# Performance work log

Measured on AMD Instinct MI355X. Metric: run time of the kernel, lower is better.

The kernel has to match this reference:

```python
import jax, jax.numpy as jnp
import numpy as np

BN_EPS = 1e-5
POOL_TARGETS = (1500, 750, 375)


def mesh_conv(x, nb, W, g, b):
    # x: (E, C), nb: (E, 4), W: (5*C, Cout)
    E, C = x.shape
    n = x[jnp.clip(nb, 0, E - 1)]              # (E, 4, C) gather
    p1 = jnp.sort(n[:, :2, :], axis=1)          # symmetrize face-pair 1
    p2 = jnp.sort(n[:, 2:, :], axis=1)          # symmetrize face-pair 2
    feat = jnp.concatenate([x, p1[:, 0], p1[:, 1], p2[:, 0], p2[:, 1]], axis=1)  # (E, 5C)
    h = feat @ W                                # (E, Cout)
    mu = h.mean(axis=0)
    var = h.var(axis=0)                         # biased var (BatchNorm training stats)
    h = (h - mu) * jax.lax.rsqrt(var + BN_EPS) * g + b
    return jax.nn.relu(h)


def mesh_pool(x, nb, target):
    E = x.shape[0]
    scores = jnp.linalg.norm(x, axis=1)
    keep = jnp.sort(jnp.argsort(-scores)[:target])          # (target,) sorted kept edges
    x_pool = x[keep]
    remap = jnp.full((E,), -1, dtype=jnp.int32).at[keep].set(jnp.arange(target, dtype=jnp.int32))
    nbr = remap[jnp.clip(nb[keep], 0, E - 1)]               # (target, 4)
    self_idx = jnp.broadcast_to(jnp.arange(target, dtype=jnp.int32)[:, None], nbr.shape)
    nb_pool = jnp.where(nbr < 0, self_idx, nbr)
    return x_pool, nb_pool, keep


def mesh_unpool(x_coarse, keep, E_fine):
    # keep is sorted ascending; nearest kept edge by integer index distance
    # (ties -> lower index, matching torch argmin-first semantics).
    idx = jnp.arange(E_fine)
    pos = jnp.searchsorted(keep, idx)
    K = keep.shape[0]
    left = jnp.clip(pos - 1, 0, K - 1)
    right = jnp.clip(pos, 0, K - 1)
    dl = jnp.abs(idx - keep[left])
    dr = jnp.abs(idx - keep[right])
    nn_idx = jnp.where(dl <= dr, left, right)
    return x_coarse[nn_idx]                                 # kept edges map to themselves (d=0)


def setup_inputs() -> dict:
    key = jax.random.key(0)
    ks = jax.random.split(key, 20)
    E = 200000
    x = jax.random.normal(ks[0], (E, 5), dtype=jnp.float32)
    nb = jax.random.randint(ks[1], (E, 4), 0, E, dtype=jnp.int64)

    def lin(k, cin, cout):
        return (jax.random.normal(k, (cin, cout), dtype=jnp.float32) * 0.05)

    dims = [(5, 64), (64, 128), (128, 256), (256, 512), (768, 256), (384, 128), (192, 64)]
    names = ['e1', 'e2', 'e3', 'e4', 'd3', 'd2', 'd1']
    inp = {'x': x, 'nb': nb}
    for i, ((cin, cout), nm) in enumerate(zip(dims, names)):
        inp['W_' + nm] = lin(ks[2 + i], cin * 5, cout)
        inp['g_' + nm] = jnp.ones((cout,), dtype=jnp.float32)
        inp['b_' + nm] = jnp.zeros((cout,), dtype=jnp.float32)
    inp['W_head'] = lin(ks[12], 64, 4)
    inp['bias_head'] = jnp.zeros((4,), dtype=jnp.float32)
    return inp


def _forward(x, nb,
             W_e1, g_e1, b_e1, W_e2, g_e2, b_e2, W_e3, g_e3, b_e3, W_e4, g_e4, b_e4,
             W_d3, g_d3, b_d3, W_d2, g_d2, b_d2, W_d1, g_d1, b_d1,
             W_head, bias_head):
    e1 = mesh_conv(x, nb, W_e1, g_e1, b_e1)
    e1p, nb1, keep1 = mesh_pool(e1, nb, POOL_TARGETS[0])
    e2 = mesh_conv(e1p, nb1, W_e2, g_e2, b_e2)
    e2p, nb2, keep2 = mesh_pool(e2, nb1, POOL_TARGETS[1])
    e3 = mesh_conv(e2p, nb2, W_e3, g_e3, b_e3)
    e3p, nb3, keep3 = mesh_pool(e3, nb2, POOL_TARGETS[2])
    e4 = mesh_conv(e3p, nb3, W_e4, g_e4, b_e4)
    d3 = mesh_unpool(e4, keep3, e3.shape[0])
    d3 = mesh_conv(jnp.concatenate([d3, e3], axis=1), nb2, W_d3, g_d3, b_d3)
    d2 = mesh_unpool(d3, keep2, e2.shape[0])
    d2 = mesh_conv(jnp.concatenate([d2, e2], axis=1), nb1, W_d2, g_d2, b_d2)
    d1 = mesh_unpool(d2, keep1, e1.shape[0])
    d1 = mesh_conv(jnp.concatenate([d1, e1], axis=1), nb, W_d1, g_d1, b_d1)
    return d1 @ W_head + bias_head


def reference(x, nb,
              W_e1, g_e1, b_e1, W_e2, g_e2, b_e2, W_e3, g_e3, b_e3, W_e4, g_e4, b_e4,
              W_d3, g_d3, b_d3, W_d2, g_d2, b_d2, W_d1, g_d1, b_d1,
              W_head, bias_head):
    return _forward(x, nb,
                    W_e1, g_e1, b_e1, W_e2, g_e2, b_e2, W_e3, g_e3, b_e3, W_e4, g_e4, b_e4,
                    W_d3, g_d3, b_d3, W_d2, g_d2, b_d2, W_d1, g_d1, b_d1,
                    W_head, bias_head)
```

## Files before the change

### kernel.cpp

```cpp
#include <hip/hip_runtime.h>
#include <stdint.h>

typedef unsigned long long u64;
typedef unsigned int u32;
typedef unsigned short ushort_t;

#define FI __device__ __forceinline__

static constexpr float BN_EPS_F = 1e-5f;
static constexpr int E0 = 200000;
static constexpr int T1 = 1500, T2 = 750, T3 = 375;
static constexpr int CAND_CAP = 4096;
static constexpr int NB_KEEP = (E0 + 1023) / 1024;

typedef __attribute__((ext_vector_type(8))) short short8;
typedef __attribute__((ext_vector_type(4))) float f32x4;

FI int iclampi(int v, int lo, int hi) { return v < lo ? lo : (v > hi ? hi : v); }

FI ushort_t f2b(float f) {
  u32 u = __float_as_uint(f);
  u32 r = (u + 0x7FFFu + ((u >> 16) & 1u)) >> 16;
  return (ushort_t)r;
}

FI int nearest_keep(const int* __restrict__ keep, int K, int idx) {
  int lo = 0, hi = K;
  while (lo < hi) { int mid = (lo + hi) >> 1; if (keep[mid] < idx) lo = mid + 1; else hi = mid; }
  int l = lo - 1; l = l < 0 ? 0 : (l > K - 1 ? K - 1 : l);
  int r = lo;     r = r < 0 ? 0 : (r > K - 1 ? K - 1 : r);
  int dl = idx - keep[l]; dl = dl < 0 ? -dl : dl;
  int dr = idx - keep[r]; dr = dr < 0 ? -dr : dr;
  return (dl <= dr) ? l : r;
}

FI int bsearch_eq(const int* __restrict__ keep, int K, int v) {
  int lo = 0, hi = K;
  while (lo < hi) { int mid = (lo + hi) >> 1; if (keep[mid] < v) lo = mid + 1; else hi = mid; }
  if (lo < K && keep[lo] == v) return lo;
  return -1;
}

template<int C, int Cout, int BR, int BC, int KT, int TR, int TC, int KSPLIT,
         bool FUSE_STATS>
__global__ __launch_bounds__((BR / TR) * (BC / TC))
void conv_kernel(const float* __restrict__ X,
                 const int* __restrict__ nb, int E,
                 const float* __restrict__ W,
                 float* __restrict__ H, float* __restrict__ stats)
{
  constexpr int NTH = (BR / TR) * (BC / TC);
  constexpr int VK = 5 * KT;
  constexpr int KC = C / KSPLIT;
  static_assert(KC % KT == 0, "KC % KT");

  const int row0 = blockIdx.x * BR;
  const int col0 = blockIdx.y * BC;
  const int c_begin = (KSPLIT > 1) ? (int)blockIdx.z * KC : 0;

  __shared__ float As[VK][BR];
  __shared__ float Bs[VK][BC];
  __shared__ int rowsS[5][BR];
  __shared__ float red[FUSE_STATS ? 2 * (BR / TR) * BC : 1];

  const int tid = threadIdx.x;

  for (int q = tid; q < BR; q += NTH) {
    int r = row0 + q;
    int rr[5];
    if (r < E) {
      rr[0] = r;
      #pragma unroll
      for (int j = 0; j < 4; j++) {
        int v = nb[(size_t)r * 4 + j];
        rr[1 + j] = iclampi(v, 0, E - 1);
      }
    } else {
      #pragma unroll
      for (int j = 0; j < 5; j++) rr[j] = -1;
    }
    #pragma unroll
    for (int j = 0; j < 5; j++) rowsS[j][q] = rr[j];
  }

  float acc[TR][TC];
  #pragma unroll
  for (int i = 0; i < TR; i++)
    #pragma unroll
    for (int j = 0; j < TC; j++) acc[i][j] = 0.f;

  const int tr = tid / (BC / TC);
  const int tc = tid % (BC / TC);
  const int rA = tr * TR;
  const int cB = tc * TC;

  for (int c0 = c_begin; c0 < c_begin + KC; c0 += KT) {
    __syncthreads();
    for (int q = tid; q < VK * (BC / 4); q += NTH) {
      int kk = q / (BC / 4);
      int c4 = q % (BC / 4);
      int p = kk / KT, t = kk % KT;
      float4 wv = *(const float4*)&W[(size_t)(p * C + c0 + t) * Cout + col0 + c4 * 4];
      *(float4*)&Bs[kk][c4 * 4] = wv;
    }
    for (int q = tid; q < BR * KT; q += NTH) {
      int t = q % KT, rq = q / KT;
      int c = c0 + t;
      float s0 = 0.f, a1 = 0.f, a2 = 0.f, a3 = 0.f, a4 = 0.f;
      if (rowsS[0][rq] >= 0) {
        float v0, v1, v2, v3;
        s0 = X[(size_t)rowsS[0][rq] * C + c];
        v0 = X[(size_t)rowsS[1][rq] * C + c];
        v1 = X[(size_t)rowsS[2][rq] * C + c];
        v2 = X[(size_t)rowsS[3][rq] * C + c];
        v3 = X[(size_t)rowsS[4][rq] * C + c];
        a1 = fminf(v0, v1); a2 = fmaxf(v0, v1);
        a3 = fminf(v2, v3); a4 = fmaxf(v2, v3);
      }
      As[0 * KT + t][rq] = s0;
      As[1 * KT + t][rq] = a1;
      As[2 * KT + t][rq] = a2;
      As[3 * KT + t][rq] = a3;
      As[4 * KT + t][rq] = a4;
    }
    __syncthreads();

    for (int kk = 0; kk < VK; kk++) {
      float a[TR], b[TC];
      #pragma unroll
      for (int i = 0; i < TR; i++) a[i] = As[kk][rA + i];
      #pragma unroll
      for (int j = 0; j < TC; j++) b[j] = Bs[kk][cB + j];
      #pragma unroll
      for (int i = 0; i < TR; i++)
        #pragma unroll
        for (int j = 0; j < TC; j++)
          acc[i][j] = fmaf(a[i], b[j], acc[i][j]);
    }
  }

  #pragma unroll
  for (int i = 0; i < TR; i++) {
    int r = row0 + rA + i;
    if (r < E) {
      if constexpr (KSPLIT > 1) {
        #pragma unroll
        for (int j = 0; j < TC; j++)
          atomicAdd(&H[(size_t)r * Cout + col0 + cB + j], acc[i][j]);
      } else {
        #pragma unroll
        for (int j = 0; j < TC; j += 4) {
          float4 v = make_float4(acc[i][j], acc[i][j + 1], acc[i][j + 2], acc[i][j + 3]);
          *(float4*)&H[(size_t)r * Cout + col0 + cB + j] = v;
        }
      }
    }
  }

  if constexpr (FUSE_STATS) {
    float s[TC], q2[TC];
    #pragma unroll
    for (int j = 0; j < TC; j++) { s[j] = 0.f; q2[j] = 0.f; }
    #pragma unroll
    for (int i = 0; i < TR; i++) {
      int r = row0 + rA + i;
      if (r < E) {
        #pragma unroll
        for (int j = 0; j < TC; j++) { float v = acc[i][j]; s[j] += v; q2[j] += v * v; }
      }
    }
    __syncthreads();
    float* redS = &red[0];
    float* redQ = &red[(BR / TR) * BC];
    #pragma unroll
    for (int j = 0; j < TC; j++) {
      redS[tr * BC + cB + j] = s[j];
      redQ[tr * BC + cB + j] = q2[j];
    }
    __syncthreads();
    for (int col = tid; col < BC; col += NTH) {
      float ts = 0.f, tq = 0.f;
      for (int g = 0; g < BR / TR; g++) { ts += redS[g * BC + col]; tq += redQ[g * BC + col]; }
      atomicAdd(&stats[col0 + col], ts);
      atomicAdd(&stats[Cout + col0 + col], tq);
    }
  }
}

__global__ __launch_bounds__(256)
void e1_conv_kernel(const float* __restrict__ X, const int* __restrict__ nb,
                    const float* __restrict__ W,
                    float* __restrict__ H, float* __restrict__ stats)
{
  __shared__ float As[25][128];
  __shared__ float Bs[25][64];
  __shared__ float red[2 * 32 * 64];

  const int tid = threadIdx.x;
  const int row0 = (int)blockIdx.x * 128;

  if (tid < 128) {
    int r = row0 + tid; if (r > E0 - 1) r = E0 - 1;
    int rs[5];
    rs[0] = r;
    #pragma unroll
    for (int j = 0; j < 4; j++) rs[1 + j] = iclampi((int)nb[(size_t)r * 4 + j], 0, E0 - 1);
    float v[5][5];
    #pragma unroll
    for (int j = 0; j < 5; j++) {
      const float* src = &X[(size_t)rs[j] * 5];
      float4 a = *(const float4*)src;
      v[j][0] = a.x; v[j][1] = a.y; v[j][2] = a.z; v[j][3] = a.w;
      v[j][4] = src[4];
    }
    #pragma unroll
    for (int c = 0; c < 5; c++) {
      As[0 * 5 + c][tid] = v[0][c];
      As[1 * 5 + c][tid] = fminf(v[1][c], v[2][c]);
      As[2 * 5 + c][tid] = fmaxf(v[1][c], v[2][c]);
      As[3 * 5 + c][tid] = fminf(v[3][c], v[4][c]);
      As[4 * 5 + c][tid] = fmaxf(v[3][c], v[4][c]);
    }
  } else {
    for (int q = tid - 128; q < 25 * 16; q += 128) {
      int k = q / 16, c4 = q % 16;
      float4 wv = *(const float4*)&W[(size_t)k * 64 + c4 * 4];
      *(float4*)&Bs[k][c4 * 4] = wv;
    }
  }
  __syncthreads();

  const int tr = tid >> 3;
  const int tc = tid & 7;
  const int rA = tr * 4;
  const int cB = tc * 8;

  float acc[4][8];
  #pragma unroll
  for (int i = 0; i < 4; i++)
    #pragma unroll
    for (int j = 0; j < 8; j++) acc[i][j] = 0.f;

  for (int k = 0; k < 25; k++) {
    float a[4], b[8];
    #pragma unroll
    for (int i = 0; i < 4; i++) a[i] = As[k][rA + i];
    #pragma unroll
    for (int j = 0; j < 8; j++) b[j] = Bs[k][cB + j];
    #pragma unroll
    for (int i = 0; i < 4; i++)
      #pragma unroll
      for (int j = 0; j < 8; j++)
        acc[i][j] = fmaf(a[i], b[j], acc[i][j]);
  }

  float s[8], q2[8];
  #pragma unroll
  for (int j = 0; j < 8; j++) { s[j] = 0.f; q2[j] = 0.f; }
  #pragma unroll
  for (int i = 0; i < 4; i++) {
    int r = row0 + rA + i;
    if (r < E0) {
      #pragma unroll
      for (int j = 0; j < 8; j += 4) {
        float4 v = make_float4(acc[i][j], acc[i][j + 1], acc[i][j + 2], acc[i][j + 3]);
        *(float4*)&H[(size_t)r * 64 + cB + j] = v;
      }
      #pragma unroll
      for (int j = 0; j < 8; j++) { float v = acc[i][j]; s[j] += v; q2[j] += v * v; }
    }
  }
  __syncthreads();
  float* redS = &red[0];
  float* redQ = &red[32 * 64];
  #pragma unroll
  for (int j = 0; j < 8; j++) {
    redS[tr * 64 + cB + j] = s[j];
    redQ[tr * 64 + cB + j] = q2[j];
  }
  __syncthreads();
  for (int col = tid; col < 64; col += 256) {
    float ts = 0.f, tq = 0.f;
    for (int g = 0; g < 32; g++) { ts += redS[g * 64 + col]; tq += redQ[g * 64 + col]; }
    atomicAdd(&stats[col], ts);
    atomicAdd(&stats[64 + col], tq);
  }
}

__global__ __launch_bounds__(256, 2)
void d1_mfma_kernel(const ushort_t* __restrict__ d2b, const ushort_t* __restrict__ e1b,
                    const int* __restrict__ nn1, const int* __restrict__ nb,
                    const ushort_t* __restrict__ Wt,
                    float* __restrict__ H, float* __restrict__ stats)
{
  __shared__ int rowsD[5][128];
  __shared__ int rowsS[5][128];

  const int tid = threadIdx.x;
  const int lane = tid & 63;
  const int wv = tid >> 6;
  const int l15 = lane & 15;
  const int quad = lane >> 4;
  const int row0 = (int)blockIdx.x * 128;

  if (tid < 128) {
    int r = row0 + tid; if (r > E0 - 1) r = E0 - 1;
    int rs[5];
    rs[0] = r;
    #pragma unroll
    for (int j = 0; j < 4; j++) rs[1 + j] = iclampi((int)nb[(size_t)r * 4 + j], 0, E0 - 1);
    #pragma unroll
    for (int j = 0; j < 5; j++) { rowsS[j][tid] = rs[j]; rowsD[j][tid] = nn1[rs[j]]; }
  }
  __syncthreads();

  f32x4 acc[2][4];
  #pragma unroll
  for (int mi = 0; mi < 2; mi++)
    #pragma unroll
    for (int ni = 0; ni < 4; ni++) acc[mi][ni] = (f32x4){0.f, 0.f, 0.f, 0.f};

  for (int cc = 0; cc < 6; cc++) {
    const bool fromD = cc < 4;
    const ushort_t* __restrict__ src = fromD ? d2b : e1b;
    const int stride = fromD ? 128 : 64;
    const int cbase = (fromD ? cc * 32 : (cc - 4) * 32) + quad * 8;

    short8 a[2][5];
    #pragma unroll
    for (int mi = 0; mi < 2; mi++) {
      int rr = wv * 32 + mi * 16 + l15;
      int r0, r1, r2, r3, r4;
      if (fromD) {
        r0 = rowsD[0][rr]; r1 = rowsD[1][rr]; r2 = rowsD[2][rr];
        r3 = rowsD[3][rr]; r4 = rowsD[4][rr];
      } else {
        r0 = rowsS[0][rr]; r1 = rowsS[1][rr]; r2 = rowsS[2][rr];
        r3 = rowsS[3][rr]; r4 = rowsS[4][rr];
      }
      uint4 v0 = *(const uint4*)&src[(size_t)r0 * stride + cbase];
      uint4 v1 = *(const uint4*)&src[(size_t)r1 * stride + cbase];
      uint4 v2 = *(const uint4*)&src[(size_t)r2 * stride + cbase];
      uint4 v3 = *(const uint4*)&src[(size_t)r3 * stride + cbase];
      uint4 v4 = *(const uint4*)&src[(size_t)r4 * stride + cbase];

      uint4 lo12, hi12, lo34, hi34;
      {
        const ushort_t* pa = (const ushort_t*)&v1;
        const ushort_t* pb = (const ushort_t*)&v2;
        ushort_t* lo = (ushort_t*)&lo12;
        ushort_t* hi = (ushort_t*)&hi12;
        #pragma unroll
        for (int i = 0; i < 8; i++) {
          ushort_t xx = pa[i], yy = pb[i];
          lo[i] = xx < yy ? xx : yy;
          hi[i] = xx < yy ? yy : xx;
        }
      }
      {
        const ushort_t* pa = (const ushort_t*)&v3;
        const ushort_t* pb = (const ushort_t*)&v4;
        ushort_t* lo = (ushort_t*)&lo34;
        ushort_t* hi = (ushort_t*)&hi34;
        #pragma unroll
        for (int i = 0; i < 8; i++) {
          ushort_t xx = pa[i], yy = pb[i];
          lo[i] = xx < yy ? xx : yy;
          hi[i] = xx < yy ? yy : xx;
        }
      }
      a[mi][0] = *(short8*)&v0;
      a[mi][1] = *(short8*)&lo12;
      a[mi][2] = *(short8*)&hi12;
      a[mi][3] = *(short8*)&lo34;
      a[mi][4] = *(short8*)&hi34;
    }

    #pragma unroll
    for (int p = 0; p < 5; p++) {
      short8 bf[4];
      #pragma unroll
      for (int ni = 0; ni < 4; ni++)
        bf[ni] = *(const short8*)&Wt[((size_t)(p * 64 + ni * 16 + l15)) * 192 + cc * 32 + quad * 8];
      #pragma unroll
      for (int mi = 0; mi < 2; mi++)
        #pragma unroll
        for (int ni = 0; ni < 4; ni++)
          acc[mi][ni] = __builtin_amdgcn_mfma_f32_16x16x32_bf16(a[mi][p], bf[ni], acc[mi][ni], 0, 0, 0);
    }
  }

  float s[4] = {0.f, 0.f, 0.f, 0.f}, q[4] = {0.f, 0.f, 0.f, 0.f};
  #pragma unroll
  for (int mi = 0; mi < 2; mi++) {
    #pragma unroll
    for (int reg = 0; reg < 4; reg++) {
      int r = row0 + wv * 32 + mi * 16 + quad * 4 + reg;
      if (r < E0) {
        #pragma unroll
        for (int ni = 0; ni < 4; ni++) {
          float v = acc[mi][ni][reg];
          H[(size_t)r * 64 + ni * 16 + l15] = v;
          s[ni] += v; q[ni] += v * v;
        }
      }
    }
  }
  #pragma unroll
  for (int ni = 0; ni < 4; ni++) {
    float ts = s[ni], tq = q[ni];
    ts += __shfl_xor(ts, 16); tq += __shfl_xor(tq, 16);
    ts += __shfl_xor(ts, 32); tq += __shfl_xor(tq, 32);
    if (quad == 0) {
      int col = ni * 16 + l15;
      atomicAdd(&stats[col], ts);
      atomicAdd(&stats[64 + col], tq);
    }
  }
}

__global__ void prep_wd1_kernel(const float* __restrict__ W, ushort_t* __restrict__ Wt)
{
  int idx = (int)blockIdx.x * 256 + threadIdx.x;
  if (idx < 5 * 64 * 192) {
    int n = idx & 63;
    int k = idx >> 6;
    int p = k / 192, c = k % 192;
    Wt[((size_t)(p * 64 + n)) * 192 + c] = f2b(W[(size_t)k * 64 + n]);
  }
}

__global__ void stats_kernel(const float* __restrict__ H, int E, int Cout,
                             float* __restrict__ stats)
{
  const int RB = 64;
  int r0 = (int)blockIdx.x * RB;
  int rend = r0 + RB; if (rend > E) rend = E;
  for (int col = threadIdx.x; col < Cout; col += blockDim.x) {
    float s = 0.f, q = 0.f;
    for (int r = r0; r < rend; r++) { float v = H[(size_t)r * Cout + col]; s += v; q += v * v; }
    atomicAdd(&stats[col], s);
    atomicAdd(&stats[Cout + col], q);
  }
}

template<int Cout, bool KEYS, bool B16>
__global__ void bn_kernel(const float* __restrict__ H, const float* __restrict__ stats,
                          const float* __restrict__ g, const float* __restrict__ b,
                          int E, float* __restrict__ Out, ushort_t* __restrict__ Outb,
                          u64* __restrict__ keys)
{
  constexpr int CPL = Cout / 64;
  const int lane = threadIdx.x & 63;
  const int wid = threadIdx.x >> 6;
  const int wpb = blockDim.x >> 6;
  const float invE = 1.0f / (float)E;
  float mu[CPL], inv[CPL], gg[CPL], bb[CPL];
  #pragma unroll
  for (int u = 0; u < CPL; u++) {
    int c = lane + u * 64;
    float m = stats[c] * invE;
    float var = stats[Cout + c] * invE - m * m;
    mu[u] = m;
    inv[u] = rsqrtf(var + BN_EPS_F);
    gg[u] = g[c]; bb[u] = b[c];
  }
  for (int r = (int)blockIdx.x * wpb + wid; r < E; r += (int)gridDim.x * wpb) {
    float ss = 0.f;
    #pragma unroll
    for (int u = 0; u < CPL; u++) {
      int c = lane + u * 64;
      float v = H[(size_t)r * Cout + c];
      float o = (v - mu[u]) * inv[u] * gg[u] + bb[u];
      o = fmaxf(o, 0.f);
      Out[(size_t)r * Cout + c] = o;
      if constexpr (B16) Outb[(size_t)r * Cout + c] = f2b(o);
      ss += o * o;
    }
    if constexpr (KEYS) {
      #pragma unroll
      for (int s = 32; s > 0; s >>= 1) ss += __shfl_xor(ss, s, 64);
      if (lane == 0) {
        float sc = sqrtf(ss);
        u32 sb = __float_as_uint(sc);
        keys[r] = ((u64)sb << 32) | (u64)(0xFFFFFFFFu - (u32)r);
      }
    }
  }
}

__global__ void head_kernel(const float* __restrict__ H, const float* __restrict__ stats,
                            const float* __restrict__ g, const float* __restrict__ b,
                            const float* __restrict__ Wh, const float* __restrict__ bh,
                            int E, float* __restrict__ out)
{
  const int lane = threadIdx.x & 63;
  const int wid = threadIdx.x >> 6;
  const int wpb = blockDim.x >> 6;
  const float invE = 1.0f / (float)E;
  float m = stats[lane] * invE;
  float var = stats[64 + lane] * invE - m * m;
  float inv = rsqrtf(var + BN_EPS_F);
  float gg = g[lane], bb = b[lane];
  float4 w = *(const float4*)&Wh[lane * 4];
  float b0 = bh[0], b1 = bh[1], b2 = bh[2], b3 = bh[3];
  for (int r = (int)blockIdx.x * wpb + wid; r < E; r += (int)gridDim.x * wpb) {
    float v = H[(size_t)r * 64 + lane];
    float o = fmaxf((v - m) * inv * gg + bb, 0.f);
    float a0 = o * w.x, a1 = o * w.y, a2 = o * w.z, a3 = o * w.w;
    #pragma unroll
    for (int s = 32; s > 0; s >>= 1) {
      a0 += __shfl_xor(a0, s, 64);
      a1 += __shfl_xor(a1, s, 64);
      a2 += __shfl_xor(a2, s, 64);
      a3 += __shfl_xor(a3, s, 64);
    }
    if (lane == 0) {
      float4 ov = make_float4(a0 + b0, a1 + b1, a2 + b2, a3 + b3);
      *(float4*)&out[(size_t)r * 4] = ov;
    }
  }
}

__global__ void hist_kernel(const u64* __restrict__ keys, int E, u32* __restrict__ hist)
{
  for (int i = (int)blockIdx.x * blockDim.x + threadIdx.x; i < E;
       i += (int)gridDim.x * blockDim.x) {
    u32 bin = (u32)(keys[i] >> 44);
    atomicAdd(&hist[bin], 1u);
  }
}

__global__ void scan_kernel(const u32* __restrict__ hist, int K, u32* __restrict__ sel)
{
  __shared__ u32 csum[1024];
  __shared__ u32 sb2[1024];
  __shared__ int selChunk;
  __shared__ u32 aboveChunk;
  const int tid = threadIdx.x;
  {
    const uint4* hp = (const uint4*)(hist + (size_t)tid * 1024);
    u32 s = 0;
    for (int i = 0; i < 256; i++) {
      uint4 v = hp[i];
      s += v.x + v.y + v.z + v.w;
    }
    csum[tid] = s;
  }
  __syncthreads();
  if (tid == 0) {
    u32 above = 0; int sc = 0; u32 ab = 0;
    for (int t = 1023; t >= 0; t--) {
      if (above + csum[t] >= (u32)K) { sc = t; ab = above; break; }
      above += csum[t];
    }
    selChunk = sc; aboveChunk = ab;
  }
  __syncthreads();
  sb2[tid] = hist[(size_t)selChunk * 1024 + tid];
  __syncthreads();
  if (tid == 0) {
    u32 above = aboveChunk; int sb = 0;
    for (int t = 1023; t >= 0; t--) {
      u32 c = sb2[t];
      if (above + c >= (u32)K) { sb = t; break; }
      above += c;
    }
    sel[0] = (u32)(selChunk * 1024 + sb);
    sel[1] = above;
    sel[2] = (u32)K - above;
  }
}

__global__ void collect_kernel(const u64* __restrict__ keys, int E, const u32* __restrict__ sel,
                               u64* __restrict__ cand, u32* __restrict__ count)
{
  u32 bin = sel[0];
  for (int i = (int)blockIdx.x * blockDim.x + threadIdx.x; i < E;
       i += (int)gridDim.x * blockDim.x) {
    if ((u32)(keys[i] >> 44) == bin) {
      u32 p = atomicAdd(count, 1u);
      if (p < (u32)CAND_CAP) cand[p] = keys[i];
    }
  }
}

__global__ void thresh_kernel(const u64* __restrict__ cand, const u32* __restrict__ count,
                              const u32* __restrict__ sel, u64* __restrict__ thr)
{
  __shared__ u64 sk[CAND_CAP];
  const int tid = threadIdx.x;
  const int nth = blockDim.x;
  int n = (int)(*count > (u32)CAND_CAP ? (u32)CAND_CAP : *count);
  int n2 = 2; while (n2 < n) n2 <<= 1;
  for (int i = tid; i < n2; i += nth) sk[i] = (i < n) ? cand[i] : 0ull;
  __syncthreads();
  for (int k = 2; k <= n2; k <<= 1)
    for (int j = k >> 1; j > 0; j >>= 1) {
      for (int i = tid; i < n2; i += nth) {
        int p = i ^ j;
        if (p > i) {
          u64 a = sk[i], bb = sk[p];
          bool up = ((i & k) == 0);
          bool sw = up ? (a < bb) : (a > bb);
          if (sw) { sk[i] = bb; sk[p] = a; }
        }
      }
      __syncthreads();
    }
  if (tid == 0) {
    int kr = (int)sel[2];
    thr[0] = sk[kr - 1];
  }
}

__global__ void keep_count_kernel(const u64* __restrict__ keys, int E,
                                  const u64* __restrict__ thrp, u32* __restrict__ bcnt)
{
  const u64 thr = thrp[0];
  const int tid = threadIdx.x;
  int base = (int)blockIdx.x * 1024 + tid * 4;
  u32 c = 0;
  #pragma unroll
  for (int u = 0; u < 4; u++) {
    int i = base + u;
    if (i < E && keys[i] >= thr) c++;
  }
  __shared__ u32 sm[256];
  sm[tid] = c;
  __syncthreads();
  for (int s = 128; s > 0; s >>= 1) {
    if (tid < s) sm[tid] += sm[tid + s];
    __syncthreads();
  }
  if (tid == 0) bcnt[blockIdx.x] = sm[0];
}

__global__ void keep_scan_kernel(const u32* __restrict__ bcnt, int NB, u32* __restrict__ boffs)
{
  __shared__ u32 sm[256];
  const int tid = threadIdx.x;
  u32 v = (tid < NB) ? bcnt[tid] : 0;
  sm[tid] = v;
  __syncthreads();
  for (int off = 1; off < 256; off <<= 1) {
    u32 t = 0;
    if (tid >= off) t = sm[tid - off];
    __syncthreads();
    sm[tid] += t;
    __syncthreads();
  }
  if (tid < NB) boffs[tid] = sm[tid] - v;
}

__global__ void keep_scatter_kernel(const u64* __restrict__ keys, int E,
                                    const u64* __restrict__ thrp, const u32* __restrict__ boffs,
                                    int* __restrict__ keep, int K)
{
  const u64 thr = thrp[0];
  const int tid = threadIdx.x;
  int base = (int)blockIdx.x * 1024 + tid * 4;
  u32 f[4]; u32 c = 0;
  #pragma unroll
  for (int u = 0; u < 4; u++) {
    int i = base + u;
    f[u] = (i < E && keys[i] >= thr) ? 1u : 0u;
    c += f[u];
  }
  __shared__ u32 sm[256];
  sm[tid] = c;
  __syncthreads();
  for (int off = 1; off < 256; off <<= 1) {
    u32 t = 0;
    if (tid >= off) t = sm[tid - off];
    __syncthreads();
    sm[tid] += t;
    __syncthreads();
  }
  u32 pos = boffs[blockIdx.x] + sm[tid] - c;
  #pragma unroll
  for (int u = 0; u < 4; u++) {
    if (f[u]) {
      if (pos < (u32)K) keep[pos] = base + u;
      pos++;
    }
  }
}

template<int NPOW>
__global__ void pool_select_kernel(const u64* __restrict__ keys, int E, int K,
                                   int* __restrict__ keep)
{
  __shared__ u64 sk[NPOW];
  __shared__ int si[NPOW];
  const int tid = threadIdx.x, nth = blockDim.x;
  for (int i = tid; i < NPOW; i += nth) sk[i] = (i < E) ? keys[i] : 0ull;
  __syncthreads();
  for (int k = 2; k <= NPOW; k <<= 1)
    for (int j = k >> 1; j > 0; j >>= 1) {
      for (int i = tid; i < NPOW; i += nth) {
        int p = i ^ j;
        if (p > i) {
          u64 a = sk[i], bb = sk[p];
          bool up = ((i & k) == 0);
          bool sw = up ? (a < bb) : (a > bb);
          if (sw) { sk[i] = bb; sk[p] = a; }
        }
      }
      __syncthreads();
    }
  for (int i = tid; i < NPOW; i += nth)
    si[i] = (i < K) ? (int)(0xFFFFFFFFu - (u32)(sk[i] & 0xFFFFFFFFull)) : 0x7FFFFFFF;
  __syncthreads();
  for (int k = 2; k <= NPOW; k <<= 1)
    for (int j = k >> 1; j > 0; j >>= 1) {
      for (int i = tid; i < NPOW; i += nth) {
        int p = i ^ j;
        if (p > i) {
          int a = si[i], bb = si[p];
          bool up = ((i & k) == 0);
          bool sw = up ? (a > bb) : (a < bb);
          if (sw) { si[i] = bb; si[p] = a; }
        }
      }
      __syncthreads();
    }
  for (int i = tid; i < K; i += nth) keep[i] = si[i];
}

template<int C>
__global__ void pool_finish_kernel(const float* __restrict__ Xsrc, const int* __restrict__ nb_src,
                                   const int* __restrict__ keep, int K, int Esrc,
                                   float* __restrict__ Xp, int* __restrict__ nbp)
{
  int total = K * C;
  for (int idx = (int)blockIdx.x * blockDim.x + threadIdx.x; idx < total;
       idx += (int)gridDim.x * blockDim.x) {
    int i = idx / C, c = idx % C;
    Xp[idx] = Xsrc[(size_t)keep[i] * C + c];
  }
  for (int idx = (int)blockIdx.x * blockDim.x + threadIdx.x; idx < K * 4;
       idx += (int)gridDim.x * blockDim.x) {
    int i = idx >> 2, j = idx & 3;
    int v = nb_src[(size_t)keep[i] * 4 + j];
    v = iclampi(v, 0, Esrc - 1);
    int p = bsearch_eq(keep, K, v);
    nbp[idx] = (p < 0) ? i : p;
  }
}

__global__ void unpool_cat_kernel(const float* __restrict__ Xc, const float* __restrict__ Xs,
                                  const int* __restrict__ keep, int K, int E,
                                  int Cc, int Cs, float* __restrict__ out)
{
  int Ct = Cc + Cs;
  int total = E * Ct;
  for (int idx = (int)blockIdx.x * blockDim.x + threadIdx.x; idx < total;
       idx += (int)gridDim.x * blockDim.x) {
    int r = idx / Ct, c = idx % Ct;
    float v;
    if (c < Cc) { int nn = nearest_keep(keep, K, r); v = Xc[(size_t)nn * Cc + c]; }
    else v = Xs[(size_t)r * Cs + (c - Cc)];
    out[idx] = v;
  }
}

__global__ void nn_map_kernel(const int* __restrict__ keep, int K, int E, int* __restrict__ nn)
{
  for (int i = (int)blockIdx.x * blockDim.x + threadIdx.x; i < E;
       i += (int)gridDim.x * blockDim.x)
    nn[i] = nearest_keep(keep, K, i);
}

extern "C" void kernel_launch(void* const* d_in, const int* in_sizes, int n_in,
                              void* d_out, int out_size, void* d_ws, size_t ws_size,
                              hipStream_t stream)
{
  (void)in_sizes; (void)n_in; (void)out_size; (void)ws_size;
  const float* x     = (const float*)d_in[0];
  const int*   nb    = (const int*)d_in[1];
  const float* W_e1  = (const float*)d_in[2];
  const float* g_e1  = (const float*)d_in[3];
  const float* b_e1  = (const float*)d_in[4];
  const float* W_e2  = (const float*)d_in[5];
  const float* g_e2  = (const float*)d_in[6];
  const float* b_e2  = (const float*)d_in[7];
  const float* W_e3  = (const float*)d_in[8];
  const float* g_e3  = (const float*)d_in[9];
  const float* b_e3  = (const float*)d_in[10];
  const float* W_e4  = (const float*)d_in[11];
  const float* g_e4  = (const float*)d_in[12];
  const float* b_e4  = (const float*)d_in[13];
  const float* W_d3  = (const float*)d_in[14];
  const float* g_d3  = (const float*)d_in[15];
  const float* b_d3  = (const float*)d_in[16];
  const float* W_d2  = (const float*)d_in[17];
  const float* g_d2  = (const float*)d_in[18];
  const float* b_d2  = (const float*)d_in[19];
  const float* W_d1  = (const float*)d_in[20];
  const float* g_d1  = (const float*)d_in[21];
  const float* b_d1  = (const float*)d_in[22];
  const float* W_head = (const float*)d_in[23];
  const float* bias_head = (const float*)d_in[24];
  float* out = (float*)d_out;

  char* p = (char*)d_ws;
  auto alloc = [&](size_t bytes) -> char* {
    char* q = p; p += (bytes + 255) & ~(size_t)255; return q;
  };

  char* zz = p;
  u32*   hist  = (u32*)alloc(sizeof(u32) * (1u << 20));
  float* stats = (float*)alloc(sizeof(float) * 2 * (64 + 128 + 256 + 512 + 256 + 128 + 64));
  u32*   ctrl  = (u32*)alloc(sizeof(u32) * 16);
  u64*   thr   = (u64*)alloc(sizeof(u64) * 2);
  u32*   sel   = (u32*)alloc(sizeof(u32) * 8);
  float* H2    = (float*)alloc(sizeof(float) * T1 * 128);
  float* H3    = (float*)alloc(sizeof(float) * T2 * 256);
  float* H4    = (float*)alloc(sizeof(float) * T3 * 512);
  float* Hd3   = (float*)alloc(sizeof(float) * T2 * 256);
  float* Hd2   = (float*)alloc(sizeof(float) * T1 * 128);
  size_t zz_bytes = (size_t)(p - zz);
  u32*   bcnt  = (u32*)alloc(sizeof(u32) * 256);
  u32*   boffs = (u32*)alloc(sizeof(u32) * 256);
  float* e1    = (float*)alloc(sizeof(float) * (size_t)E0 * 64);
  u64*   keys1 = (u64*)alloc(sizeof(u64) * E0);
  u64*   cand  = (u64*)alloc(sizeof(u64) * CAND_CAP);
  int*   keep1 = (int*)alloc(sizeof(int) * T1);
  float* e1p   = (float*)alloc(sizeof(float) * T1 * 64);
  int*   nb1   = (int*)alloc(sizeof(int) * T1 * 4);
  float* e2    = (float*)alloc(sizeof(float) * T1 * 128);
  u64*   keys2 = (u64*)alloc(sizeof(u64) * T1);
  int*   keep2 = (int*)alloc(sizeof(int) * T2);
  float* e2p   = (float*)alloc(sizeof(float) * T2 * 128);
  int*   nb2   = (int*)alloc(sizeof(int) * T2 * 4);
  float* e3    = (float*)alloc(sizeof(float) * T2 * 256);
  u64*   keys3 = (u64*)alloc(sizeof(u64) * T2);
  int*   keep3 = (int*)alloc(sizeof(int) * T3);
  float* e3p   = (float*)alloc(sizeof(float) * T3 * 256);
  int*   nb3   = (int*)alloc(sizeof(int) * T3 * 4);
  float* e4    = (float*)alloc(sizeof(float) * T3 * 512);
  float* d3cat = (float*)alloc(sizeof(float) * T2 * 768);
  float* d3    = (float*)alloc(sizeof(float) * T2 * 256);
  float* d2cat = (float*)alloc(sizeof(float) * T1 * 384);
  float* d2    = (float*)alloc(sizeof(float) * T1 * 128);
  int*   nn1   = (int*)alloc(sizeof(int) * E0);
  float* Hd1   = (float*)alloc(sizeof(float) * (size_t)E0 * 64);
  ushort_t* e1b = (ushort_t*)alloc(sizeof(ushort_t) * (size_t)E0 * 64);
  ushort_t* d2b = (ushort_t*)alloc(sizeof(ushort_t) * T1 * 128);
  ushort_t* Wt  = (ushort_t*)alloc(sizeof(ushort_t) * 5 * 64 * 192);

  float* s1  = stats;
  float* s2  = s1 + 2 * 64;
  float* s3  = s2 + 2 * 128;
  float* s4  = s3 + 2 * 256;
  float* sd3 = s4 + 2 * 512;
  float* sd2 = sd3 + 2 * 256;
  float* sd1 = sd2 + 2 * 128;

  hipMemsetAsync(zz, 0, zz_bytes, stream);
  prep_wd1_kernel<<<dim3(240), 256, 0, stream>>>(W_d1, Wt);

  e1_conv_kernel<<<dim3((E0 + 127) / 128), 256, 0, stream>>>(x, nb, W_e1, e1, s1);
  bn_kernel<64, true, true><<<dim3(8192), 256, 0, stream>>>(e1, s1, g_e1, b_e1, E0, e1, e1b, keys1);

  hist_kernel<<<dim3(782), 256, 0, stream>>>(keys1, E0, hist);
  scan_kernel<<<dim3(1), 1024, 0, stream>>>(hist, T1, sel);
  collect_kernel<<<dim3(782), 256, 0, stream>>>(keys1, E0, sel, cand, ctrl);
  thresh_kernel<<<dim3(1), 1024, 0, stream>>>(cand, ctrl, sel, thr);
  keep_count_kernel<<<dim3(NB_KEEP), 256, 0, stream>>>(keys1, E0, thr, bcnt);
  keep_scan_kernel<<<dim3(1), 256, 0, stream>>>(bcnt, NB_KEEP, boffs);
  keep_scatter_kernel<<<dim3(NB_KEEP), 256, 0, stream>>>(keys1, E0, thr, boffs, keep1, T1);
  pool_finish_kernel<64><<<dim3(380), 256, 0, stream>>>(e1, nb, keep1, T1, E0, e1p, nb1);

  conv_kernel<64, 128, 32, 64, 8, 2, 4, 2, false>
      <<<dim3((T1 + 31) / 32, 128 / 64, 2), 256, 0, stream>>>(e1p, nb1, T1, W_e2, H2, nullptr);
  stats_kernel<<<dim3((T1 + 63) / 64), 256, 0, stream>>>(H2, T1, 128, s2);
  bn_kernel<128, true, false><<<dim3(512), 256, 0, stream>>>(H2, s2, g_e2, b_e2, T1, e2, nullptr, keys2);
  pool_select_kernel<2048><<<dim3(1), 256, 0, stream>>>(keys2, T1, T2, keep2);
  pool_finish_kernel<128><<<dim3(380), 256, 0, stream>>>(e2, nb1, keep2, T2, T1, e2p, nb2);

  conv_kernel<128, 256, 32, 64, 8, 2, 4, 4, false>
      <<<dim3((T2 + 31) / 32, 256 / 64, 4), 256, 0, stream>>>(e2p, nb2, T2, W_e3, H3, nullptr);
  stats_kernel<<<dim3((T2 + 63) / 64), 256, 0, stream>>>(H3, T2, 256, s3);
  bn_kernel<256, true, false><<<dim3(256), 256, 0, stream>>>(H3, s3, g_e3, b_e3, T2, e3, nullptr, keys3);
  pool_select_kernel<1024><<<dim3(1), 256, 0, stream>>>(keys3, T2, T3, keep3);
  pool_finish_kernel<256><<<dim3(380), 256, 0, stream>>>(e3, nb2, keep3, T3, T2, e3p, nb3);

  conv_kernel<256, 512, 32, 64, 8, 2, 4, 4, false>
      <<<dim3((T3 + 31) / 32, 512 / 64, 4), 256, 0, stream>>>(e3p, nb3, T3, W_e4, H4, nullptr);
  stats_kernel<<<dim3((T3 + 63) / 64), 256, 0, stream>>>(H4, T3, 512, s4);
  bn_kernel<512, false, false><<<dim3(128), 256, 0, stream>>>(H4, s4, g_e4, b_e4, T3, e4, nullptr, nullptr);

  unpool_cat_kernel<<<dim3((T2 * 768 + 255) / 256), 256, 0, stream>>>(
      e4, e3, keep3, T3, T2, 512, 256, d3cat);
  conv_kernel<768, 256, 32, 64, 8, 2, 4, 8, false>
      <<<dim3((T2 + 31) / 32, 256 / 64, 8), 256, 0, stream>>>(d3cat, nb2, T2, W_d3, Hd3, nullptr);
  stats_kernel<<<dim3((T2 + 63) / 64), 256, 0, stream>>>(Hd3, T2, 256, sd3);
  bn_kernel<256, false, false><<<dim3(256), 256, 0, stream>>>(Hd3, sd3, g_d3, b_d3, T2, d3, nullptr, nullptr);

  unpool_cat_kernel<<<dim3((T1 * 384 + 255) / 256), 256, 0, stream>>>(
      d3, e2, keep2, T2, T1, 256, 128, d2cat);
  conv_kernel<384, 128, 32, 64, 8, 2, 4, 8, false>
      <<<dim3((T1 + 31) / 32, 128 / 64, 8), 256, 0, stream>>>(d2cat, nb1, T1, W_d2, Hd2, nullptr);
  stats_kernel<<<dim3((T1 + 63) / 64), 256, 0, stream>>>(Hd2, T1, 128, sd2);
  bn_kernel<128, false, true><<<dim3(512), 256, 0, stream>>>(Hd2, sd2, g_d2, b_d2, T1, d2, d2b, nullptr);

  nn_map_kernel<<<dim3(782), 256, 0, stream>>>(keep1, T1, E0, nn1);
  d1_mfma_kernel<<<dim3((E0 + 127) / 128), 256, 0, stream>>>(d2b, e1b, nn1, nb, Wt, Hd1, sd1);

  head_kernel<<<dim3(8192), 256, 0, stream>>>(Hd1, sd1, g_d1, b_d1, W_head, bias_head, E0, out);
}
```

Baseline: 1.194 ms.

## Move e4/d3/d2 convs to bf16 MFMA kernel with fused stats; prefetch d1 gathers

Adds a templated bf16 MFMA mesh-conv kernel that gathers bf16 rows, symmetrises neighbour pairs with u16 min/max and accumulates per-column BN statistics in the epilogue. It replaces the fp32 split-K conv plus separate stats kernels for e4, d3 and d2. Pool-finish and unpool-concat now write bf16 inputs, and new prep kernels transpose and convert those weights. The d1 kernel double-buffers its gathered rows so the next chunk loads while the current one computes. The cost is extra weight-conversion launches per call, bf16 rounding on these layers, and no split-K, so the small-E layers get fewer blocks.

```diff
diff --git a/kernel.cpp b/kernel.cpp
--- a/kernel.cpp
+++ b/kernel.cpp
@@ -22,6 +22,19 @@
   u32 u = __float_as_uint(f);
   u32 r = (u + 0x7FFFu + ((u >> 16) & 1u)) >> 16;
   return (ushort_t)r;
+}
+
+FI void u16minmax(const uint4& va, const uint4& vb, uint4& lo, uint4& hi) {
+  const ushort_t* a = (const ushort_t*)&va;
+  const ushort_t* b = (const ushort_t*)&vb;
+  ushort_t* l = (ushort_t*)&lo;
+  ushort_t* h = (ushort_t*)&hi;
+  #pragma unroll
+  for (int i = 0; i < 8; i++) {
+    ushort_t x = a[i], y = b[i];
+    l[i] = x < y ? x : y;
+    h[i] = x < y ? y : x;
+  }
 }
 
 FI int nearest_keep(const int* __restrict__ keep, int K, int idx) {
@@ -287,6 +300,102 @@
   }
 }
 
+template<int C, int Cout>
+__global__ __launch_bounds__(128)
+void mfma_conv_kernel(const ushort_t* __restrict__ src,
+                      const int* __restrict__ nb, int E,
+                      const ushort_t* __restrict__ Wt,
+                      float* __restrict__ H, float* __restrict__ stats)
+{
+  constexpr int NCC = C / 32;
+  __shared__ int rows[5][32];
+
+  const int tid = threadIdx.x;
+  const int lane = tid & 63;
+  const int wv = tid >> 6;
+  const int l15 = lane & 15;
+  const int quad = lane >> 4;
+  const int row0 = (int)blockIdx.x * 32;
+  const int col0 = (int)blockIdx.y * 64;
+
+  if (tid < 32) {
+    int r = row0 + tid; if (r > E - 1) r = E - 1;
+    rows[0][tid] = r;
+    #pragma unroll
+    for (int j = 0; j < 4; j++) rows[1 + j][tid] = iclampi(nb[(size_t)r * 4 + j], 0, E - 1);
+  }
+  __syncthreads();
+
+  const int rr = wv * 16 + l15;
+  int r5[5];
+  #pragma unroll
+  for (int j = 0; j < 5; j++) r5[j] = rows[j][rr];
+
+  f32x4 acc[4];
+  #pragma unroll
+  for (int ni = 0; ni < 4; ni++) acc[ni] = (f32x4){0.f, 0.f, 0.f, 0.f};
+
+  uint4 raw[2][5];
+  auto loadcc = [&](int par, int cc2) {
+    int cb = cc2 * 32 + quad * 8;
+    #pragma unroll
+    for (int j = 0; j < 5; j++)
+      raw[par][j] = *(const uint4*)&src[(size_t)r5[j] * C + cb];
+  };
+
+  loadcc(0, 0);
+  #pragma unroll
+  for (int cc = 0; cc < NCC; cc++) {
+    const int par = cc & 1;
+    if (cc + 1 < NCC) loadcc(par ^ 1, cc + 1);
+    short8 a[5];
+    a[0] = *(short8*)&raw[par][0];
+    {
+      uint4 lo, hi;
+      u16minmax(raw[par][1], raw[par][2], lo, hi);
+      a[1] = *(short8*)&lo; a[2] = *(short8*)&hi;
+    }
+    {
+      uint4 lo, hi;
+      u16minmax(raw[par][3], raw[par][4], lo, hi);
+      a[3] = *(short8*)&lo; a[4] = *(short8*)&hi;
+    }
+    #pragma unroll
+    for (int p = 0; p < 5; p++) {
+      #pragma unroll
+      for (int ni = 0; ni < 4; ni++) {
+        short8 bf = *(const short8*)&Wt[((size_t)(p * Cout + col0 + ni * 16 + l15)) * C + cc * 32 + quad * 8];
+        acc[ni] = __builtin_amdgcn_mfma_f32_16x16x32_bf16(a[p], bf, acc[ni], 0, 0, 0);
+      }
+    }
+  }
+
+  float s[4] = {0.f, 0.f, 0.f, 0.f}, q[4] = {0.f, 0.f, 0.f, 0.f};
+  #pragma unroll
+  for (int reg = 0; reg < 4; reg++) {
+    int r = row0 + wv * 16 + quad * 4 + reg;
+    if (r < E) {
+      #pragma unroll
+      for (int ni = 0; ni < 4; ni++) {
+        float v = acc[ni][reg];
+        H[(size_t)r * Cout + col0 + ni * 16 + l15] = v;
+        s[ni] += v; q[ni] += v * v;
+      }
+    }
+  }
+  #pragma unroll
+  for (int ni = 0; ni < 4; ni++) {
+    float ts = s[ni], tq = q[ni];
+    ts += __shfl_xor(ts, 16); tq += __shfl_xor(tq, 16);
+    ts += __shfl_xor(ts, 32); tq += __shfl_xor(tq, 32);
+    if (quad == 0) {
+      int col = col0 + ni * 16 + l15;
+      atomicAdd(&stats[col], ts);
+      atomicAdd(&stats[Cout + col], tq);
+    }
+  }
+}
+
 __global__ __launch_bounds__(256, 2)
 void d1_mfma_kernel(const ushort_t* __restrict__ d2b, const ushort_t* __restrict__ e1b,
                     const int* __restrict__ nn1, const int* __restrict__ nb,
@@ -314,68 +423,55 @@
   }
   __syncthreads();
 
+  int rD[2][5], rS[2][5];
+  #pragma unroll
+  for (int mi = 0; mi < 2; mi++) {
+    int rr = wv * 32 + mi * 16 + l15;
+    #pragma unroll
+    for (int j = 0; j < 5; j++) { rD[mi][j] = rowsD[j][rr]; rS[mi][j] = rowsS[j][rr]; }
+  }
+
   f32x4 acc[2][4];
   #pragma unroll
   for (int mi = 0; mi < 2; mi++)
     #pragma unroll
     for (int ni = 0; ni < 4; ni++) acc[mi][ni] = (f32x4){0.f, 0.f, 0.f, 0.f};
 
+  uint4 raw[2][2][5];
+  auto loadcc = [&](int par, int cc2) {
+    const bool fD = cc2 < 4;
+    const ushort_t* s2 = fD ? d2b : e1b;
+    const int st = fD ? 128 : 64;
+    const int cb = (fD ? cc2 * 32 : (cc2 - 4) * 32) + quad * 8;
+    #pragma unroll
+    for (int mi = 0; mi < 2; mi++)
+      #pragma unroll
+      for (int j = 0; j < 5; j++) {
+        int r = fD ? rD[mi][j] : rS[mi][j];
+        raw[par][mi][j] = *(const uint4*)&s2[(size_t)r * st + cb];
+      }
+  };
+
+  loadcc(0, 0);
+  #pragma unroll
   for (int cc = 0; cc < 6; cc++) {
-    const bool fromD = cc < 4;
-    const ushort_t* __restrict__ src = fromD ? d2b : e1b;
-    const int stride = fromD ? 128 : 64;
-    const int cbase = (fromD ? cc * 32 : (cc - 4) * 32) + quad * 8;
-
+    const int par = cc & 1;
+    if (cc + 1 < 6) loadcc(par ^ 1, cc + 1);
     short8 a[2][5];
     #pragma unroll
     for (int mi = 0; mi < 2; mi++) {
-      int rr = wv * 32 + mi * 16 + l15;
-      int r0, r1, r2, r3, r4;
-      if (fromD) {
-        r0 = rowsD[0][rr]; r1 = rowsD[1][rr]; r2 = rowsD[2][rr];
-        r3 = rowsD[3][rr]; r4 = rowsD[4][rr];
-      } else {
-        r0 = rowsS[0][rr]; r1 = rowsS[1][rr]; r2 = rowsS[2][rr];
-        r3 = rowsS[3][rr]; r4 = rowsS[4][rr];
-      }
-      uint4 v0 = *(const uint4*)&src[(size_t)r0 * stride + cbase];
-      uint4 v1 = *(const uint4*)&src[(size_t)r1 * stride + cbase];
-      uint4 v2 = *(const uint4*)&src[(size_t)r2 * stride + cbase];
-      uint4 v3 = *(const uint4*)&src[(size_t)r3 * stride + cbase];
-      uint4 v4 = *(const uint4*)&src[(size_t)r4 * stride + cbase];
-
-      uint4 lo12, hi12, lo34, hi34;
+      a[mi][0] = *(short8*)&raw[par][mi][0];
       {
-        const ushort_t* pa = (const ushort_t*)&v1;
-        const ushort_t* pb = (const ushort_t*)&v2;
-        ushort_t* lo = (ushort_t*)&lo12;
-        ushort_t* hi = (ushort_t*)&hi12;
-        #pragma unroll
-        for (int i = 0; i < 8; i++) {
-          ushort_t xx = pa[i], yy = pb[i];
-          lo[i] = xx < yy ? xx : yy;
-          hi[i] = xx < yy ? yy : xx;
-        }
+        uint4 lo, hi;
+        u16minmax(raw[par][mi][1], raw[par][mi][2], lo, hi);
+        a[mi][1] = *(short8*)&lo; a[mi][2] = *(short8*)&hi;
       }
       {
-        const ushort_t* pa = (const ushort_t*)&v3;
-        const ushort_t* pb = (const ushort_t*)&v4;
-        ushort_t* lo = (ushort_t*)&lo34;
-        ushort_t* hi = (ushort_t*)&hi34;
-        #pragma unroll
-        for (int i = 0; i < 8; i++) {
-          ushort_t xx = pa[i], yy = pb[i];
-          lo[i] = xx < yy ? xx : yy;
-          hi[i] = xx < yy ? yy : xx;
-        }
-      }
-      a[mi][0] = *(short8*)&v0;
-      a[mi][1] = *(short8*)&lo12;
-      a[mi][2] = *(short8*)&hi12;
-      a[mi][3] = *(short8*)&lo34;
-      a[mi][4] = *(short8*)&hi34;
-    }
-
+        uint4 lo, hi;
+        u16minmax(raw[par][mi][3], raw[par][mi][4], lo, hi);
+        a[mi][3] = *(short8*)&lo; a[mi][4] = *(short8*)&hi;
+      }
+    }
     #pragma unroll
     for (int p = 0; p < 5; p++) {
       short8 bf[4];
@@ -419,14 +515,15 @@
   }
 }
 
-__global__ void prep_wd1_kernel(const float* __restrict__ W, ushort_t* __restrict__ Wt)
+template<int C, int Cout>
+__global__ void prep_w_kernel(const float* __restrict__ W, ushort_t* __restrict__ Wt)
 {
   int idx = (int)blockIdx.x * 256 + threadIdx.x;
-  if (idx < 5 * 64 * 192) {
-    int n = idx & 63;
-    int k = idx >> 6;
-    int p = k / 192, c = k % 192;
-    Wt[((size_t)(p * 64 + n)) * 192 + c] = f2b(W[(size_t)k * 64 + n]);
+  if (idx < 5 * C * Cout) {
+    int n = idx % Cout;
+    int k = idx / Cout;
+    int p = k / C, c = k % C;
+    Wt[((size_t)(p * Cout + n)) * C + c] = f2b(W[(size_t)k * Cout + n]);
   }
 }
 
@@ -728,16 +825,19 @@
   for (int i = tid; i < K; i += nth) keep[i] = si[i];
 }
 
-template<int C>
+template<int C, bool B16>
 __global__ void pool_finish_kernel(const float* __restrict__ Xsrc, const int* __restrict__ nb_src,
                                    const int* __restrict__ keep, int K, int Esrc,
-                                   float* __restrict__ Xp, int* __restrict__ nbp)
+                                   float* __restrict__ Xp, ushort_t* __restrict__ Xpb,
+                                   int* __restrict__ nbp)
 {
   int total = K * C;
   for (int idx = (int)blockIdx.x * blockDim.x + threadIdx.x; idx < total;
        idx += (int)gridDim.x * blockDim.x) {
     int i = idx / C, c = idx % C;
-    Xp[idx] = Xsrc[(size_t)keep[i] * C + c];
+    float v = Xsrc[(size_t)keep[i] * C + c];
+    if constexpr (B16) Xpb[idx] = f2b(v);
+    else Xp[idx] = v;
   }
   for (int idx = (int)blockIdx.x * blockDim.x + threadIdx.x; idx < K * 4;
        idx += (int)gridDim.x * blockDim.x) {
@@ -749,9 +849,9 @@
   }
 }
 
-__global__ void unpool_cat_kernel(const float* __restrict__ Xc, const float* __restrict__ Xs,
-                                  const int* __restrict__ keep, int K, int E,
-                                  int Cc, int Cs, float* __restrict__ out)
+__global__ void unpool_cat_b16_kernel(const float* __restrict__ Xc, const float* __restrict__ Xs,
+                                      const int* __restrict__ keep, int K, int E,
+                                      int Cc, int Cs, ushort_t* __restrict__ out)
 {
   int Ct = Cc + Cs;
   int total = E * Ct;
@@ -761,7 +861,7 @@
     float v;
     if (c < Cc) { int nn = nearest_keep(keep, K, r); v = Xc[(size_t)nn * Cc + c]; }
     else v = Xs[(size_t)r * Cs + (c - Cc)];
-    out[idx] = v;
+    out[idx] = f2b(v);
   }
 }
 
@@ -817,10 +917,10 @@
   u32*   sel   = (u32*)alloc(sizeof(u32) * 8);
   float* H2    = (float*)alloc(sizeof(float) * T1 * 128);
   float* H3    = (float*)alloc(sizeof(float) * T2 * 256);
+  size_t zz_bytes = (size_t)(p - zz);
   float* H4    = (float*)alloc(sizeof(float) * T3 * 512);
   float* Hd3   = (float*)alloc(sizeof(float) * T2 * 256);
   float* Hd2   = (float*)alloc(sizeof(float) * T1 * 128);
-  size_t zz_bytes = (size_t)(p - zz);
   u32*   bcnt  = (u32*)alloc(sizeof(u32) * 256);
   u32*   boffs = (u32*)alloc(sizeof(u32) * 256);
   float* e1    = (float*)alloc(sizeof(float) * (size_t)E0 * 64);
@@ -837,18 +937,21 @@
   float* e3    = (float*)alloc(sizeof(float) * T2 * 256);
   u64*   keys3 = (u64*)alloc(sizeof(u64) * T2);
   int*   keep3 = (int*)alloc(sizeof(int) * T3);
-  float* e3p   = (float*)alloc(sizeof(float) * T3 * 256);
+  ushort_t* e3pb = (ushort_t*)alloc(sizeof(ushort_t) * T3 * 256);
   int*   nb3   = (int*)alloc(sizeof(int) * T3 * 4);
   float* e4    = (float*)alloc(sizeof(float) * T3 * 512);
-  float* d3cat = (float*)alloc(sizeof(float) * T2 * 768);
+  ushort_t* d3catb = (ushort_t*)alloc(sizeof(ushort_t) * T2 * 768);
   float* d3    = (float*)alloc(sizeof(float) * T2 * 256);
-  float* d2cat = (float*)alloc(sizeof(float) * T1 * 384);
+  ushort_t* d2catb = (ushort_t*)alloc(sizeof(ushort_t) * T1 * 384);
   float* d2    = (float*)alloc(sizeof(float) * T1 * 128);
   int*   nn1   = (int*)alloc(sizeof(int) * E0);
   float* Hd1   = (float*)alloc(sizeof(float) * (size_t)E0 * 64);
   ushort_t* e1b = (ushort_t*)alloc(sizeof(ushort_t) * (size_t)E0 * 64);
   ushort_t* d2b = (ushort_t*)alloc(sizeof(ushort_t) * T1 * 128);
-  ushort_t* Wt  = (ushort_t*)alloc(sizeof(ushort_t) * 5 * 64 * 192);
+  ushort_t* Wt1 = (ushort_t*)alloc(sizeof(ushort_t) * 5 * 64 * 192);
+  ushort_t* Wt4 = (ushort_t*)alloc(sizeof(ushort_t) * 5 * 512 * 256);
+  ushort_t* Wtd3 = (ushort_t*)alloc(sizeof(ushort_t) * 5 * 256 * 768);
+  ushort_t* Wtd2 = (ushort_t*)alloc(sizeof(ushort_t) * 5 * 128 * 384);
 
   float* s1  = stats;
   float* s2  = s1 + 2 * 64;
@@ -859,7 +962,10 @@
   float* sd1 = sd2 + 2 * 128;
 
   hipMemsetAsync(zz, 0, zz_bytes, stream);
-  prep_wd1_kernel<<<dim3(240), 256, 0, stream>>>(W_d1, Wt);
+  prep_w_kernel<192, 64><<<dim3((5 * 192 * 64 + 255) / 256), 256, 0, stream>>>(W_d1, Wt1);
+  prep_w_kernel<256, 512><<<dim3((5 * 256 * 512 + 255) / 256), 256, 0, stream>>>(W_e4, Wt4);
+  prep_w_kernel<768, 256><<<dim3((5 * 768 * 256 + 255) / 256), 256, 0, stream>>>(W_d3, Wtd3);
+  prep_w_kernel<384, 128><<<dim3((5 * 384 * 128 + 255) / 256), 256, 0, stream>>>(W_d2, Wtd2);
 
   e1_conv_kernel<<<dim3((E0 + 127) / 128), 256, 0, stream>>>(x, nb, W_e1, e1, s1);
   bn_kernel<64, true, true><<<dim3(8192), 256, 0, stream>>>(e1, s1, g_e1, b_e1, E0, e1, e1b, keys1);
@@ -871,43 +977,40 @@
   keep_count_kernel<<<dim3(NB_KEEP), 256, 0, stream>>>(keys1, E0, thr, bcnt);
   keep_scan_kernel<<<dim3(1), 256, 0, stream>>>(bcnt, NB_KEEP, boffs);
   keep_scatter_kernel<<<dim3(NB_KEEP), 256, 0, stream>>>(keys1, E0, thr, boffs, keep1, T1);
-  pool_finish_kernel<64><<<dim3(380), 256, 0, stream>>>(e1, nb, keep1, T1, E0, e1p, nb1);
+  pool_finish_kernel<64, false><<<dim3(380), 256, 0, stream>>>(e1, nb, keep1, T1, E0, e1p, nullptr, nb1);
 
   conv_kernel<64, 128, 32, 64, 8, 2, 4, 2, false>
       <<<dim3((T1 + 31) / 32, 128 / 64, 2), 256, 0, stream>>>(e1p, nb1, T1, W_e2, H2, nullptr);
   stats_kernel<<<dim3((T1 + 63) / 64), 256, 0, stream>>>(H2, T1, 128, s2);
   bn_kernel<128, true, false><<<dim3(512), 256, 0, stream>>>(H2, s2, g_e2, b_e2, T1, e2, nullptr, keys2);
   pool_select_kernel<2048><<<dim3(1), 256, 0, stream>>>(keys2, T1, T2, keep2);
-  pool_finish_kernel<128><<<dim3(380), 256, 0, stream>>>(e2, nb1, keep2, T2, T1, e2p, nb2);
+  pool_finish_kernel<128, false><<<dim3(380), 256, 0, stream>>>(e2, nb1, keep2, T2, T1, e2p, nullptr, nb2);
 
   conv_kernel<128, 256, 32, 64, 8, 2, 4, 4, false>
       <<<dim3((T2 + 31) / 32, 256 / 64, 4), 256, 0, stream>>>(e2p, nb2, T2, W_e3, H3, nullptr);
   stats_kernel<<<dim3((T2 + 63) / 64), 256, 0, stream>>>(H3, T2, 256, s3);
   bn_kernel<256, true, false><<<dim3(256), 256, 0, stream>>>(H3, s3, g_e3, b_e3, T2, e3, nullptr, keys3);
   pool_select_kernel<1024><<<dim3(1), 256, 0, stream>>>(keys3, T2, T3, keep3);
-  pool_finish_kernel<256><<<dim3(380), 256, 0, stream>>>(e3, nb2, keep3, T3, T2, e3p, nb3);
-
-  conv_kernel<256, 512, 32, 64, 8, 2, 4, 4, false>
-      <<<dim3((T3 + 31) / 32, 512 / 64, 4), 256, 0, stream>>>(e3p, nb3, T3, W_e4, H4, nullptr);
-  stats_kernel<<<dim3((T3 + 63) / 64), 256, 0, stream>>>(H4, T3, 512, s4);
+  pool_finish_kernel<256, true><<<dim3(380), 256, 0, stream>>>(e3, nb2, keep3, T3, T2, nullptr, e3pb, nb3);
+
+  mfma_conv_kernel<256, 512><<<dim3((T3 + 31) / 32, 512 / 64), 128, 0, stream>>>(
+      e3pb, nb3, T3, Wt4, H4, s4);
   bn_kernel<512, false, false><<<dim3(128), 256, 0, stream>>>(H4, s4, g_e4, b_e4, T3, e4, nullptr, nullptr);
 
-  unpool_cat_kernel<<<dim3((T2 * 768 + 255) / 256), 256, 0, stream>>>(
-      e4, e3, keep3, T3, T2, 512, 256, d3cat);
-  conv_kernel<768, 256, 32, 64, 8, 2, 4, 8, false>
-      <<<dim3((T2 + 31) / 32, 256 / 64, 8), 256, 0, stream>>>(d3cat, nb2, T2, W_d3, Hd3, nullptr);
-  stats_kernel<<<dim3((T2 + 63) / 64), 256, 0, stream>>>(Hd3, T2, 256, sd3);
+  unpool_cat_b16_kernel<<<dim3((T2 * 768 + 255) / 256), 256, 0, stream>>>(
+      e4, e3, keep3, T3, T2, 512, 256, d3catb);
+  mfma_conv_kernel<768, 256><<<dim3((T2 + 31) / 32, 256 / 64), 128, 0, stream>>>(
+      d3catb, nb2, T2, Wtd3, Hd3, sd3);
   bn_kernel<256, false, false><<<dim3(256), 256, 0, stream>>>(Hd3, sd3, g_d3, b_d3, T2, d3, nullptr, nullptr);
 
-  unpool_cat_kernel<<<dim3((T1 * 384 + 255) / 256), 256, 0, stream>>>(
-      d3, e2, keep2, T2, T1, 256, 128, d2cat);
-  conv_kernel<384, 128, 32, 64, 8, 2, 4, 8, false>
-      <<<dim3((T1 + 31) / 32, 128 / 64, 8), 256, 0, stream>>>(d2cat, nb1, T1, W_d2, Hd2, nullptr);
-  stats_kernel<<<dim3((T1 + 63) / 64), 256, 0, stream>>>(Hd2, T1, 128, sd2);
+  unpool_cat_b16_kernel<<<dim3((T1 * 384 + 255) / 256), 256, 0, stream>>>(
+      d3, e2, keep2, T2, T1, 256, 128, d2catb);
+  mfma_conv_kernel<384, 128><<<dim3((T1 + 31) / 32, 128 / 64), 128, 0, stream>>>(
+      d2catb, nb1, T1, Wtd2, Hd2, sd2);
   bn_kernel<128, false, true><<<dim3(512), 256, 0, stream>>>(Hd2, sd2, g_d2, b_d2, T1, d2, d2b, nullptr);
 
   nn_map_kernel<<<dim3(782), 256, 0, stream>>>(keep1, T1, E0, nn1);
-  d1_mfma_kernel<<<dim3((E0 + 127) / 128), 256, 0, stream>>>(d2b, e1b, nn1, nb, Wt, Hd1, sd1);
+  d1_mfma_kernel<<<dim3((E0 + 127) / 128), 256, 0, stream>>>(d2b, e1b, nn1, nb, Wt1, Hd1, sd1);
 
   head_kernel<<<dim3(8192), 256, 0, stream>>>(Hd1, sd1, g_d1, b_d1, W_head, bias_head, E0, out);
 }
```

Result: faster. 1.139 ms (-4.6%).
